# Performance work log

Measured on AMD Instinct MI355X. Metric: run time of the kernel, lower is better.

## Reference

```python
import jax, jax.numpy as jnp
import numpy as np

B, T, L = 64, 512, 48
START, PAD, END = 46, 45, 47


def setup_inputs() -> dict:
    key = jax.random.key(0)
    k1, k2, k3 = jax.random.split(key, 3)
    scores = jax.random.normal(k1, (B, T, L), dtype=jnp.float32)
    gold_target = jax.random.randint(k2, (B, T), 0, L, dtype=jnp.int64)
    trans = jax.random.normal(k3, (L, L), dtype=jnp.float32)
    # replicate the in-place constraint initialization from __init__ (order matters)
    trans = trans.at[:, START].set(-10000.0)
    trans = trans.at[END, :].set(-10000.0)
    trans = trans.at[PAD, :].set(-10000.0)
    trans = trans.at[PAD, END].set(0.0)
    trans = trans.at[PAD, PAD].set(0.0)
    trans = trans.at[START, :].set(0.0)
    mask = jnp.ones((B, T), dtype=jnp.int32)
    return {"scores": scores, "gold_target": gold_target, "mask": mask, "transitions": trans}


def reference(scores, gold_target, mask, transitions):
    Bn, Tn, Ln = scores.shape
    # crf_scores[t, b, from, to] = emission(b, t, from) + transitions[from, to]  (time-major)
    crf = scores.transpose(1, 0, 2)[:, :, :, None] + transitions[None, None]      # (T, B, L, L)
    start = jnp.broadcast_to(transitions[None, None], (1, Bn, Ln, Ln))
    crf = jnp.concatenate([start, crf], axis=0)                                   # (T+1, B, L, L)

    # gold energy: faithful to original torch.gather on flattened (L*L) with raw tag index
    gold = jnp.concatenate(
        [jnp.full((1, Bn), START, dtype=gold_target.dtype), gold_target.T], axis=0)  # (T+1, B)
    flat = crf.reshape(Tn + 1, Bn, Ln * Ln)
    tg = jnp.take_along_axis(flat, gold[:, :, None], axis=2)[:, :, 0]             # (T+1, B)
    maskp = jnp.concatenate([jnp.ones((1, Bn), mask.dtype), mask.T], axis=0)      # (T+1, B)
    tg_energy = jnp.sum(tg * maskp.astype(tg.dtype))

    # forward algorithm (stable log-sum-exp recurrence) via lax.scan
    init = crf[0, :, START, :]                                                    # (B, L)
    def step(fs, xs):
        trans_t, m_t = xs                                                         # (B,L,L), (B,)
        nxt = jax.nn.logsumexp(fs[:, :, None] + trans_t, axis=1)                  # (B, L)
        fs = jnp.where(m_t[:, None].astype(bool), nxt, fs)
        return fs, None
    fs, _ = jax.lax.scan(step, init, (crf[1:], maskp[1:]))
    forscore = fs[:, END].sum()

    return (forscore - tg_energy) / Bn
```

## Files before the change

kernel.cpp:

```cpp
#include <hip/hip_runtime.h>

#define Bn 64
#define Tn 512
#define Ln 48
#define START_L 46
#define PAD_L 45
#define END_L 47
#define QP 72
#define LSEG 16
#define NSEG 8
#define NCHUNK (Tn / (LSEG * NSEG))

typedef __bf16 bf16x8 __attribute__((ext_vector_type(8)));
typedef float f32x4 __attribute__((ext_vector_type(4)));
#define MFMA __builtin_amdgcn_mfma_f32_16x16x32_bf16

__device__ __forceinline__ unsigned short f2bf(float x) {
    unsigned u = __float_as_uint(x);
    u += 0x7fffu + ((u >> 16) & 1u);
    return (unsigned short)(u >> 16);
}
__device__ __forceinline__ unsigned pkT(float a, float b) {
    return __builtin_amdgcn_perm(__float_as_uint(b), __float_as_uint(a), 0x07060302u);
}
__device__ __forceinline__ float bcast0(float x) {
    return __int_as_float(__builtin_amdgcn_readfirstlane(__float_as_int(x)));
}
__device__ __forceinline__ float4 exp4(float4 v) {
    float4 r; r.x = __expf(v.x); r.y = __expf(v.y); r.z = __expf(v.z); r.w = __expf(v.w);
    return r;
}


__device__ __forceinline__ void readTB(const unsigned short* buf, int c, int q, bf16x8 F[3][2]) {
    #pragma unroll
    for (int x = 0; x < 3; ++x) {
        F[x][0] = *(const bf16x8*)&buf[(x * 16 + c) * QP + q * 8];
        F[x][1] = *(const bf16x8*)&buf[(x * 16 + c) * QP + 32 + q * 8];
    }
}

__device__ __forceinline__ void storeTB(unsigned short* buf, int c, int q,
                                        const f32x4 (&acc)[3][3],
                                        float4 w0, float4 w1, float4 w2) {
    #pragma unroll
    for (int nt = 0; nt < 3; ++nt) {
        unsigned u0 = pkT(acc[0][nt][0] * w0.x, acc[0][nt][1] * w0.y);
        unsigned u1 = pkT(acc[0][nt][2] * w0.z, acc[0][nt][3] * w0.w);
        unsigned u2 = pkT(acc[1][nt][0] * w1.x, acc[1][nt][1] * w1.y);
        unsigned u3 = pkT(acc[1][nt][2] * w1.z, acc[1][nt][3] * w1.w);
        unsigned u4 = pkT(acc[2][nt][0] * w2.x, acc[2][nt][1] * w2.y);
        unsigned u5 = pkT(acc[2][nt][2] * w2.z, acc[2][nt][3] * w2.w);
        unsigned short* wp = &buf[(nt * 16 + c) * QP + q * 16];
        uint4 s4; s4.x = u0; s4.y = u1; s4.z = u2; s4.w = u3;
        *(uint4*)wp = s4;
        uint2 s2; s2.x = u4; s2.y = u5;
        *(uint2*)(wp + 8) = s2;
    }
}

__device__ __forceinline__ float treeProd(const unsigned short* bufA, const unsigned short* bufB,
                                          unsigned short* dst, int c, int q) {
    bf16x8 FA[3][2], FB[3][2];
    readTB(bufA, c, q, FA);
    readTB(bufB, c, q, FB);
    f32x4 acc[3][3];
    const f32x4 z = {0.f, 0.f, 0.f, 0.f};
    #pragma unroll
    for (int mt = 0; mt < 3; ++mt)
        #pragma unroll
        for (int nt = 0; nt < 3; ++nt) {
            acc[mt][nt] = MFMA(FA[mt][0], FB[nt][0], z, 0, 0, 0);
            acc[mt][nt] = MFMA(FA[mt][1], FB[nt][1], acc[mt][nt], 0, 0, 0);
        }
    float r = bcast0(acc[0][0][0]);
    float rr = __builtin_amdgcn_rcpf(r);
    float4 w; w.x = rr; w.y = rr; w.z = rr; w.w = rr;
    storeTB(dst, c, q, acc, w, w, w);
    return __logf(r);
}

__global__ __launch_bounds__(512, 2) void scan_k(
        const float* __restrict__ scores,
        const float* __restrict__ trans,
        unsigned short* __restrict__ ws2M,
        float* __restrict__ ws2S,
        float* __restrict__ out) {
    const int b   = blockIdx.x & (Bn - 1);
    const int cid = blockIdx.x >> 6;
    const int tid = threadIdx.x;
    const int w   = tid >> 6;
    const int lane = tid & 63;
    const int c = lane & 15;
    const int q = lane >> 4;

    __shared__ __align__(16) unsigned short TBs[NSEG][48 * QP];
    __shared__ float scl[16];

    for (int i = tid; i < NSEG * 48 * QP / 4; i += 512)
        ((unsigned long long*)TBs)[i] = 0ull;
    __syncthreads();

    const int s    = cid * NSEG + w;
    const int t0   = s * LSEG;
    const int tend = t0 + LSEG - 1;
    const int dirOdd = w & 1;
    const float* sb = scores + (size_t)b * Tn * Ln;

    bf16x8 A[3][2];
    #pragma unroll
    for (int mt = 0; mt < 3; ++mt)
        #pragma unroll
        for (int kt = 0; kt < 2; ++kt) {
            union { unsigned u[4]; bf16x8 v; } fu;
            #pragma unroll
            for (int j2 = 0; j2 < 4; ++j2) {
                int kk0 = kt * 32 + q * 8 + 2 * j2;
                int rem = kk0 & 15;
                if (rem < 12) {
                    int row0 = (rem >> 2) * 16 + (kk0 >> 4) * 4 + (kk0 & 3);
                    float tv0 = dirOdd ? trans[(mt * 16 + c) * Ln + row0]
                                       : trans[row0 * Ln + mt * 16 + c];
                    float tv1 = dirOdd ? trans[(mt * 16 + c) * Ln + row0 + 1]
                                       : trans[(row0 + 1) * Ln + mt * 16 + c];
                    fu.u[j2] = pkT(__expf(tv0), __expf(tv1));
                } else fu.u[j2] = 0u;
            }
            A[mt][kt] = fu.v;
        }

    unsigned short* myTB = TBs[w];

    if (lane < Ln) {
        int m16 = lane >> 4, q4 = (lane >> 2) & 3, r = lane & 3;
        int kk = q4 * 16 + m16 * 4 + r;
        myTB[lane * QP + kk] = dirOdd ? (unsigned short)0x3F80
                                      : f2bf(__expf(sb[(size_t)t0 * Ln + lane]));
    }

    float4 wA, wB, wC, rA, rB, rC;
    {
        int t1 = dirOdd ? tend : (t0 + 1);
        const float* rp = sb + (size_t)t1 * Ln;
        wA = exp4(*(const float4*)(rp + q * 4));
        wB = exp4(*(const float4*)(rp + 16 + q * 4));
        wC = exp4(*(const float4*)(rp + 32 + q * 4));
        int t2 = dirOdd ? (tend - 1) : (t0 + 2);
        const float* rp2 = sb + (size_t)t2 * Ln;
        rA = *(const float4*)(rp2 + q * 4);
        rB = *(const float4*)(rp2 + 16 + q * 4);
        rC = *(const float4*)(rp2 + 32 + q * 4);
    }

    f32x4 acc[3][3];
    float Cs = 0.f;
    for (int tau = 0; tau < LSEG; ++tau) {
        bf16x8 Bf[3][2];
        readTB(myTB, c, q, Bf);

        int tp = dirOdd ? (tend - (tau + 2)) : (t0 + 3 + tau);
        if (tp < t0) tp = t0;
        if (tp > tend) tp = tend;
        const float* rp3 = sb + (size_t)tp * Ln;
        float4 nA = *(const float4*)(rp3 + q * 4);
        float4 nB = *(const float4*)(rp3 + 16 + q * 4);
        float4 nC = *(const float4*)(rp3 + 32 + q * 4);

        const f32x4 z = {0.f, 0.f, 0.f, 0.f};
        #pragma unroll
        for (int mt = 0; mt < 3; ++mt)
            #pragma unroll
            for (int nt = 0; nt < 3; ++nt) {
                acc[mt][nt] = MFMA(A[mt][0], Bf[nt][0], z, 0, 0, 0);
                acc[mt][nt] = MFMA(A[mt][1], Bf[nt][1], acc[mt][nt], 0, 0, 0);
            }

        float4 w0 = wA, w1 = wB, w2 = wC;
        if (!dirOdd && tau == LSEG - 1) {
            w0.x = w0.y = w0.z = w0.w = 1.f; w1 = w0; w2 = w0;
        }
        if ((tau & 3) == 0) {
            float r = bcast0(acc[0][0][0]);
            float rr = __builtin_amdgcn_rcpf(r);
            Cs += __logf(r);
            w0.x *= rr; w0.y *= rr; w0.z *= rr; w0.w *= rr;
            w1.x *= rr; w1.y *= rr; w1.z *= rr; w1.w *= rr;
            w2.x *= rr; w2.y *= rr; w2.z *= rr; w2.w *= rr;
        }
        storeTB(myTB, c, q, acc, w0, w1, w2);

        wA = exp4(rA); wB = exp4(rB); wC = exp4(rC);
        rA = nA; rB = nB; rC = nC;
    }
    if (lane == 0) scl[w] = Cs;
    __syncthreads();

    if (w < 4) {
        const unsigned short* bufA = TBs[(w & 1) ? (2 * w) : (2 * w + 1)];
        const unsigned short* bufB = TBs[(w & 1) ? (2 * w + 1) : (2 * w)];
        float lg = treeProd(bufA, bufB, TBs[2 * w], c, q);
        if (lane == 0) scl[8 + w] = lg;
    }
    __syncthreads();
    if (w < 2) {
        const unsigned short* bufA = TBs[w ? 4 : 2];
        const unsigned short* bufB = TBs[w ? 6 : 0];
        float lg = treeProd(bufA, bufB, TBs[w ? 4 : 0], c, q);
        if (lane == 0) scl[12 + w] = lg;
    }
    __syncthreads();
    if (w == 0) {
        bf16x8 FA[3][2], FB[3][2];
        readTB(TBs[4], c, q, FA);
        readTB(TBs[0], c, q, FB);
        f32x4 pac[3][3];
        const f32x4 z = {0.f, 0.f, 0.f, 0.f};
        #pragma unroll
        for (int mt = 0; mt < 3; ++mt)
            #pragma unroll
            for (int nt = 0; nt < 3; ++nt) {
                pac[mt][nt] = MFMA(FA[mt][0], FB[nt][0], z, 0, 0, 0);
                pac[mt][nt] = MFMA(FA[mt][1], FB[nt][1], pac[mt][nt], 0, 0, 0);
            }
        float r = bcast0(pac[0][0][0]);
        float rr = __builtin_amdgcn_rcpf(r);
        float Ct = __logf(r);
        #pragma unroll
        for (int i2 = 0; i2 < 14; ++i2) Ct += scl[i2];
        unsigned short* mp = ws2M + (size_t)blockIdx.x * (Ln * Ln);
        #pragma unroll
        for (int mt = 0; mt < 3; ++mt)
            #pragma unroll
            for (int nt = 0; nt < 3; ++nt)
                #pragma unroll
                for (int r2 = 0; r2 < 4; ++r2)
                    mp[(mt * 16 + q * 4 + r2) * Ln + nt * 16 + c] = f2bf(pac[mt][nt][r2] * rr);
        if (lane == 0) ws2S[blockIdx.x] = Ct;
    }
    if (blockIdx.x == 0 && tid == 0) out[0] = 0.f;
}

__global__ __launch_bounds__(64) void fin_k(
        const float* __restrict__ scores,
        const int* __restrict__ gold,
        const int* __restrict__ mask,
        const float* __restrict__ trans,
        const unsigned short* __restrict__ ws2M,
        const float* __restrict__ ws2S,
        float* __restrict__ out) {
    const int b = blockIdx.x;
    const int lane = threadIdx.x;
    const int j = (lane < Ln) ? lane : (Ln - 1);

    __shared__ float vB[64];

    float v = (lane < Ln) ? __expf(trans[START_L * Ln + lane]) : 0.0f;
    float Ctot = 0.0f;

    uint4 rows[NCHUNK][6];
    #pragma unroll
    for (int s2 = 0; s2 < NCHUNK; ++s2) {
        const unsigned short* p = ws2M + (size_t)(s2 * Bn + b) * (Ln * Ln) + (size_t)j * Ln;
        #pragma unroll
        for (int k = 0; k < 6; ++k) rows[s2][k] = *(const uint4*)(p + k * 8);
    }

    #pragma unroll
    for (int s2 = 0; s2 < NCHUNK; ++s2) {
        float Cs = ws2S[s2 * Bn + b];
        if (lane < Ln) vB[lane] = v;

        float a0 = 0.f, a1 = 0.f, a2 = 0.f, a3 = 0.f;
        #pragma unroll
        for (int k2 = 0; k2 < 12; ++k2) {
            float4 vb = *(const float4*)&vB[k2 * 4];
            uint4 ch = rows[s2][k2 >> 1];
            unsigned d0 = (k2 & 1) ? ch.z : ch.x;
            unsigned d1 = (k2 & 1) ? ch.w : ch.y;
            float f0 = __uint_as_float(d0 << 16);
            float f1 = __uint_as_float(d0 & 0xffff0000u);
            float f2 = __uint_as_float(d1 << 16);
            float f3 = __uint_as_float(d1 & 0xffff0000u);
            a0 = fmaf(f0, vb.x, a0);
            a1 = fmaf(f1, vb.y, a1);
            a2 = fmaf(f2, vb.z, a2);
            a3 = fmaf(f3, vb.w, a3);
        }
        float accv = (a0 + a1) + (a2 + a3);

        float r = bcast0(accv);
        v = accv * __builtin_amdgcn_rcpf(r);
        Ctot += __logf(r) + Cs;
    }

    if (lane == END_L) {
        atomicAdd(out, (__logf(v) + Ctot) * (1.0f / Bn));
    }

    float tgv = 0.0f;
    #pragma unroll
    for (int k = 0; k < Tn / 64; ++k) {
        int t = lane + k * 64;
        int idx = b * Tn + t;
        if (mask[idx]) tgv += scores[(size_t)idx * Ln] + trans[gold[idx]];
    }
    #pragma unroll
    for (int off = 32; off > 0; off >>= 1) tgv += __shfl_down(tgv, off);
    if (lane == 0) {
        float vv = -tgv * (1.0f / Bn);
        if (b == 0) vv -= trans[START_L];
        atomicAdd(out, vv);
    }
}

extern "C" void kernel_launch(void* const* d_in, const int* in_sizes, int n_in,
                              void* d_out, int out_size, void* d_ws, size_t ws_size,
                              hipStream_t stream) {
    const float* scores = (const float*)d_in[0];
    const int*   gold   = (const int*)d_in[1];
    const int*   mask   = (const int*)d_in[2];
    const float* trans  = (const float*)d_in[3];
    float* out = (float*)d_out;

    unsigned short* ws2M = (unsigned short*)d_ws;
    float* ws2S = (float*)((char*)d_ws + (size_t)Bn * NCHUNK * Ln * Ln * 2);

    scan_k<<<Bn * NCHUNK, 512, 0, stream>>>(scores, trans, ws2M, ws2S, out);
    fin_k<<<Bn, 64, 0, stream>>>(scores, gold, mask, trans, ws2M, ws2S, out);
}
```

Measured before the change: 85.43 us.

## Add prep kernel to precompute exponentiated emissions, transition fragments and gold terms

```diff
diff --git a/kernel.cpp b/kernel.cpp
--- a/kernel.cpp
+++ b/kernel.cpp
@@ -15,6 +15,11 @@
 typedef float f32x4 __attribute__((ext_vector_type(4)));
 #define MFMA __builtin_amdgcn_mfma_f32_16x16x32_bf16
 
+#define OFF_2M (6291456)
+#define OFF_A  (OFF_2M + 1179648)
+#define OFF_G  (OFF_A + 12288)
+#define OFF_2S (OFF_G + 131072)
+
 __device__ __forceinline__ unsigned short f2bf(float x) {
     unsigned u = __float_as_uint(x);
     u += 0x7fffu + ((u >> 16) & 1u);
@@ -29,6 +34,56 @@
 __device__ __forceinline__ float4 exp4(float4 v) {
     float4 r; r.x = __expf(v.x); r.y = __expf(v.y); r.z = __expf(v.z); r.w = __expf(v.w);
     return r;
+}
+
+__global__ __launch_bounds__(256) void prep_k(
+        const float* __restrict__ scores,
+        const int* __restrict__ gold,
+        const float* __restrict__ trans,
+        float* __restrict__ wsE,
+        float* __restrict__ wsG,
+        uint4* __restrict__ wsA,
+        float* __restrict__ out) {
+    const int gid = blockIdx.x * 256 + threadIdx.x;
+    const int gsz = gridDim.x * 256;
+
+    const int N4 = Bn * Tn * Ln / 4;
+    for (int i = gid; i < N4; i += gsz) {
+        float4 v = ((const float4*)scores)[i];
+        ((float4*)wsE)[i] = exp4(v);
+    }
+
+    for (int i = gid; i < Bn * Tn; i += gsz) {
+        wsG[i] = scores[(size_t)i * Ln] + trans[gold[i]];
+    }
+
+    if (blockIdx.x == 0) {
+        for (int e = threadIdx.x; e < 768; e += 256) {
+            int lane = e & 63;
+            int kt   = (e >> 6) & 1;
+            int mt   = (e >> 7) % 3;
+            int dir  = e >= 384;
+            int c = lane & 15, q = lane >> 4;
+            uint4 val;
+            unsigned uu[4];
+            #pragma unroll
+            for (int j2 = 0; j2 < 4; ++j2) {
+                int kk0 = kt * 32 + q * 8 + 2 * j2;
+                int rem = kk0 & 15;
+                if (rem < 12) {
+                    int row0 = (rem >> 2) * 16 + (kk0 >> 4) * 4 + (kk0 & 3);
+                    float tv0 = dir ? trans[(mt * 16 + c) * Ln + row0]
+                                    : trans[row0 * Ln + mt * 16 + c];
+                    float tv1 = dir ? trans[(mt * 16 + c) * Ln + row0 + 1]
+                                    : trans[(row0 + 1) * Ln + mt * 16 + c];
+                    uu[j2] = pkT(__expf(tv0), __expf(tv1));
+                } else uu[j2] = 0u;
+            }
+            val.x = uu[0]; val.y = uu[1]; val.z = uu[2]; val.w = uu[3];
+            wsA[e] = val;
+        }
+        if (threadIdx.x == 255) out[0] = 0.0f;
+    }
 }
 
 
@@ -81,11 +136,10 @@
 }
 
 __global__ __launch_bounds__(512, 2) void scan_k(
-        const float* __restrict__ scores,
-        const float* __restrict__ trans,
+        const float* __restrict__ wsE,
+        const uint4* __restrict__ wsA,
         unsigned short* __restrict__ ws2M,
-        float* __restrict__ ws2S,
-        float* __restrict__ out) {
+        float* __restrict__ ws2S) {
     const int b   = blockIdx.x & (Bn - 1);
     const int cid = blockIdx.x >> 6;
     const int tid = threadIdx.x;
@@ -105,29 +159,20 @@
     const int t0   = s * LSEG;
     const int tend = t0 + LSEG - 1;
     const int dirOdd = w & 1;
-    const float* sb = scores + (size_t)b * Tn * Ln;
+    const float* eb = wsE + (size_t)b * Tn * Ln;
 
     bf16x8 A[3][2];
-    #pragma unroll
-    for (int mt = 0; mt < 3; ++mt)
-        #pragma unroll
-        for (int kt = 0; kt < 2; ++kt) {
-            union { unsigned u[4]; bf16x8 v; } fu;
-            #pragma unroll
-            for (int j2 = 0; j2 < 4; ++j2) {
-                int kk0 = kt * 32 + q * 8 + 2 * j2;
-                int rem = kk0 & 15;
-                if (rem < 12) {
-                    int row0 = (rem >> 2) * 16 + (kk0 >> 4) * 4 + (kk0 & 3);
-                    float tv0 = dirOdd ? trans[(mt * 16 + c) * Ln + row0]
-                                       : trans[row0 * Ln + mt * 16 + c];
-                    float tv1 = dirOdd ? trans[(mt * 16 + c) * Ln + row0 + 1]
-                                       : trans[(row0 + 1) * Ln + mt * 16 + c];
-                    fu.u[j2] = pkT(__expf(tv0), __expf(tv1));
-                } else fu.u[j2] = 0u;
+    {
+        const uint4* ap = wsA + (dirOdd ? 384 : 0) + lane;
+        #pragma unroll
+        for (int mt = 0; mt < 3; ++mt)
+            #pragma unroll
+            for (int kt = 0; kt < 2; ++kt) {
+                union { uint4 u; bf16x8 v; } fu;
+                fu.u = ap[(mt * 2 + kt) * 64];
+                A[mt][kt] = fu.v;
             }
-            A[mt][kt] = fu.v;
-        }
+    }
 
     unsigned short* myTB = TBs[w];
 
@@ -135,18 +180,18 @@
         int m16 = lane >> 4, q4 = (lane >> 2) & 3, r = lane & 3;
         int kk = q4 * 16 + m16 * 4 + r;
         myTB[lane * QP + kk] = dirOdd ? (unsigned short)0x3F80
-                                      : f2bf(__expf(sb[(size_t)t0 * Ln + lane]));
+                                      : f2bf(eb[(size_t)t0 * Ln + lane]);
     }
 
     float4 wA, wB, wC, rA, rB, rC;
     {
         int t1 = dirOdd ? tend : (t0 + 1);
-        const float* rp = sb + (size_t)t1 * Ln;
-        wA = exp4(*(const float4*)(rp + q * 4));
-        wB = exp4(*(const float4*)(rp + 16 + q * 4));
-        wC = exp4(*(const float4*)(rp + 32 + q * 4));
+        const float* rp = eb + (size_t)t1 * Ln;
+        wA = *(const float4*)(rp + q * 4);
+        wB = *(const float4*)(rp + 16 + q * 4);
+        wC = *(const float4*)(rp + 32 + q * 4);
         int t2 = dirOdd ? (tend - 1) : (t0 + 2);
-        const float* rp2 = sb + (size_t)t2 * Ln;
+        const float* rp2 = eb + (size_t)t2 * Ln;
         rA = *(const float4*)(rp2 + q * 4);
         rB = *(const float4*)(rp2 + 16 + q * 4);
         rC = *(const float4*)(rp2 + 32 + q * 4);
@@ -161,7 +206,7 @@
         int tp = dirOdd ? (tend - (tau + 2)) : (t0 + 3 + tau);
         if (tp < t0) tp = t0;
         if (tp > tend) tp = tend;
-        const float* rp3 = sb + (size_t)tp * Ln;
+        const float* rp3 = eb + (size_t)tp * Ln;
         float4 nA = *(const float4*)(rp3 + q * 4);
         float4 nB = *(const float4*)(rp3 + 16 + q * 4);
         float4 nC = *(const float4*)(rp3 + 32 + q * 4);
@@ -189,7 +234,7 @@
         }
         storeTB(myTB, c, q, acc, w0, w1, w2);
 
-        wA = exp4(rA); wB = exp4(rB); wC = exp4(rC);
+        wA = rA; wB = rB; wC = rC;
         rA = nA; rB = nB; rC = nC;
     }
     if (lane == 0) scl[w] = Cs;
@@ -237,16 +282,14 @@
                     mp[(mt * 16 + q * 4 + r2) * Ln + nt * 16 + c] = f2bf(pac[mt][nt][r2] * rr);
         if (lane == 0) ws2S[blockIdx.x] = Ct;
     }
-    if (blockIdx.x == 0 && tid == 0) out[0] = 0.f;
 }
 
 __global__ __launch_bounds__(64) void fin_k(
-        const float* __restrict__ scores,
-        const int* __restrict__ gold,
         const int* __restrict__ mask,
         const float* __restrict__ trans,
         const unsigned short* __restrict__ ws2M,
         const float* __restrict__ ws2S,
+        const float* __restrict__ wsG,
         float* __restrict__ out) {
     const int b = blockIdx.x;
     const int lane = threadIdx.x;
@@ -300,9 +343,8 @@
     float tgv = 0.0f;
     #pragma unroll
     for (int k = 0; k < Tn / 64; ++k) {
-        int t = lane + k * 64;
-        int idx = b * Tn + t;
-        if (mask[idx]) tgv += scores[(size_t)idx * Ln] + trans[gold[idx]];
+        int idx = b * Tn + lane + k * 64;
+        if (mask[idx]) tgv += wsG[idx];
     }
     #pragma unroll
     for (int off = 32; off > 0; off >>= 1) tgv += __shfl_down(tgv, off);
@@ -322,9 +364,14 @@
     const float* trans  = (const float*)d_in[3];
     float* out = (float*)d_out;
 
-    unsigned short* ws2M = (unsigned short*)d_ws;
-    float* ws2S = (float*)((char*)d_ws + (size_t)Bn * NCHUNK * Ln * Ln * 2);
-
-    scan_k<<<Bn * NCHUNK, 512, 0, stream>>>(scores, trans, ws2M, ws2S, out);
-    fin_k<<<Bn, 64, 0, stream>>>(scores, gold, mask, trans, ws2M, ws2S, out);
-}
+    char* base = (char*)d_ws;
+    float*          wsE  = (float*)base;
+    unsigned short* ws2M = (unsigned short*)(base + OFF_2M);
+    uint4*          wsA  = (uint4*)(base + OFF_A);
+    float*          wsG  = (float*)(base + OFF_G);
+    float*          ws2S = (float*)(base + OFF_2S);
+
+    prep_k<<<512, 256, 0, stream>>>(scores, gold, trans, wsE, wsG, wsA, out);
+    scan_k<<<Bn * NCHUNK, 512, 0, stream>>>(wsE, wsA, ws2M, ws2S);
+    fin_k<<<Bn, 64, 0, stream>>>(mask, trans, ws2M, ws2S, wsG, out);
+}
```

Measured after the change: 88.97 us. 4.1% more time.

## Interleave two independent segment chains per wave with shorter segments

Applied to the files above, without the earlier changes.

```diff
diff --git a/kernel.cpp b/kernel.cpp
--- a/kernel.cpp
+++ b/kernel.cpp
@@ -7,9 +7,9 @@
 #define PAD_L 45
 #define END_L 47
 #define QP 72
-#define LSEG 16
-#define NSEG 8
-#define NCHUNK (Tn / (LSEG * NSEG))
+#define LSEG 8
+#define NBUF 16
+#define NCHUNK (Tn / (LSEG * NBUF))
 
 typedef __bf16 bf16x8 __attribute__((ext_vector_type(8)));
 typedef float f32x4 __attribute__((ext_vector_type(4)));
@@ -94,17 +94,18 @@
     const int c = lane & 15;
     const int q = lane >> 4;
 
-    __shared__ __align__(16) unsigned short TBs[NSEG][48 * QP];
-    __shared__ float scl[16];
-
-    for (int i = tid; i < NSEG * 48 * QP / 4; i += 512)
+    __shared__ __align__(16) unsigned short TBs[NBUF][48 * QP];
+    __shared__ float scl[32];
+
+    for (int i = tid; i < NBUF * 48 * QP / 4; i += 512)
         ((unsigned long long*)TBs)[i] = 0ull;
     __syncthreads();
 
-    const int s    = cid * NSEG + w;
-    const int t0   = s * LSEG;
-    const int tend = t0 + LSEG - 1;
     const int dirOdd = w & 1;
+    const int s1 = cid * NBUF + w;
+    const int s2 = s1 + 8;
+    const int t0a = s1 * LSEG, tea = t0a + LSEG - 1;
+    const int t0b = s2 * LSEG, teb = t0b + LSEG - 1;
     const float* sb = scores + (size_t)b * Tn * Ln;
 
     bf16x8 A[3][2];
@@ -129,89 +130,130 @@
             A[mt][kt] = fu.v;
         }
 
-    unsigned short* myTB = TBs[w];
+    unsigned short* TB0 = TBs[w];
+    unsigned short* TB1 = TBs[w + 8];
 
     if (lane < Ln) {
         int m16 = lane >> 4, q4 = (lane >> 2) & 3, r = lane & 3;
         int kk = q4 * 16 + m16 * 4 + r;
-        myTB[lane * QP + kk] = dirOdd ? (unsigned short)0x3F80
-                                      : f2bf(__expf(sb[(size_t)t0 * Ln + lane]));
-    }
-
-    float4 wA, wB, wC, rA, rB, rC;
+        TB0[lane * QP + kk] = dirOdd ? (unsigned short)0x3F80
+                                     : f2bf(__expf(sb[(size_t)t0a * Ln + lane]));
+        TB1[lane * QP + kk] = dirOdd ? (unsigned short)0x3F80
+                                     : f2bf(__expf(sb[(size_t)t0b * Ln + lane]));
+    }
+
+    auto clampA = [&](int t) { return t < t0a ? t0a : (t > tea ? tea : t); };
+    auto clampB = [&](int t) { return t < t0b ? t0b : (t > teb ? teb : t); };
+
+    float4 wA0, wA1, wA2, wB0, wB1, wB2;
     {
-        int t1 = dirOdd ? tend : (t0 + 1);
-        const float* rp = sb + (size_t)t1 * Ln;
-        wA = exp4(*(const float4*)(rp + q * 4));
-        wB = exp4(*(const float4*)(rp + 16 + q * 4));
-        wC = exp4(*(const float4*)(rp + 32 + q * 4));
-        int t2 = dirOdd ? (tend - 1) : (t0 + 2);
-        const float* rp2 = sb + (size_t)t2 * Ln;
-        rA = *(const float4*)(rp2 + q * 4);
-        rB = *(const float4*)(rp2 + 16 + q * 4);
-        rC = *(const float4*)(rp2 + 32 + q * 4);
-    }
-
-    f32x4 acc[3][3];
-    float Cs = 0.f;
+        const float* rp = sb + (size_t)(dirOdd ? tea : (t0a + 1)) * Ln;
+        wA0 = exp4(*(const float4*)(rp + q * 4));
+        wA1 = exp4(*(const float4*)(rp + 16 + q * 4));
+        wA2 = exp4(*(const float4*)(rp + 32 + q * 4));
+        const float* rp2 = sb + (size_t)(dirOdd ? teb : (t0b + 1)) * Ln;
+        wB0 = exp4(*(const float4*)(rp2 + q * 4));
+        wB1 = exp4(*(const float4*)(rp2 + 16 + q * 4));
+        wB2 = exp4(*(const float4*)(rp2 + 32 + q * 4));
+    }
+
+    f32x4 acc0[3][3], acc1[3][3];
+    float Cs0 = 0.f, Cs1 = 0.f;
     for (int tau = 0; tau < LSEG; ++tau) {
-        bf16x8 Bf[3][2];
-        readTB(myTB, c, q, Bf);
-
-        int tp = dirOdd ? (tend - (tau + 2)) : (t0 + 3 + tau);
-        if (tp < t0) tp = t0;
-        if (tp > tend) tp = tend;
-        const float* rp3 = sb + (size_t)tp * Ln;
-        float4 nA = *(const float4*)(rp3 + q * 4);
-        float4 nB = *(const float4*)(rp3 + 16 + q * 4);
-        float4 nC = *(const float4*)(rp3 + 32 + q * 4);
+        bf16x8 Bf0[3][2], Bf1[3][2];
+        readTB(TB0, c, q, Bf0);
+        readTB(TB1, c, q, Bf1);
+
+        int tnA = clampA(dirOdd ? (tea - (tau + 1)) : (t0a + 2 + tau));
+        int tnB = clampB(dirOdd ? (teb - (tau + 1)) : (t0b + 2 + tau));
+        const float* rpA = sb + (size_t)tnA * Ln;
+        const float* rpB = sb + (size_t)tnB * Ln;
+        float4 nA0 = *(const float4*)(rpA + q * 4);
+        float4 nA1 = *(const float4*)(rpA + 16 + q * 4);
+        float4 nA2 = *(const float4*)(rpA + 32 + q * 4);
+        float4 nB0 = *(const float4*)(rpB + q * 4);
+        float4 nB1 = *(const float4*)(rpB + 16 + q * 4);
+        float4 nB2 = *(const float4*)(rpB + 32 + q * 4);
 
         const f32x4 z = {0.f, 0.f, 0.f, 0.f};
         #pragma unroll
         for (int mt = 0; mt < 3; ++mt)
             #pragma unroll
             for (int nt = 0; nt < 3; ++nt) {
-                acc[mt][nt] = MFMA(A[mt][0], Bf[nt][0], z, 0, 0, 0);
-                acc[mt][nt] = MFMA(A[mt][1], Bf[nt][1], acc[mt][nt], 0, 0, 0);
-            }
-
-        float4 w0 = wA, w1 = wB, w2 = wC;
-        if (!dirOdd && tau == LSEG - 1) {
-            w0.x = w0.y = w0.z = w0.w = 1.f; w1 = w0; w2 = w0;
-        }
-        if ((tau & 3) == 0) {
-            float r = bcast0(acc[0][0][0]);
-            float rr = __builtin_amdgcn_rcpf(r);
-            Cs += __logf(r);
-            w0.x *= rr; w0.y *= rr; w0.z *= rr; w0.w *= rr;
-            w1.x *= rr; w1.y *= rr; w1.z *= rr; w1.w *= rr;
-            w2.x *= rr; w2.y *= rr; w2.z *= rr; w2.w *= rr;
-        }
-        storeTB(myTB, c, q, acc, w0, w1, w2);
-
-        wA = exp4(rA); wB = exp4(rB); wC = exp4(rC);
-        rA = nA; rB = nB; rC = nC;
-    }
-    if (lane == 0) scl[w] = Cs;
-    __syncthreads();
-
+                acc0[mt][nt] = MFMA(A[mt][0], Bf0[nt][0], z, 0, 0, 0);
+                acc0[mt][nt] = MFMA(A[mt][1], Bf0[nt][1], acc0[mt][nt], 0, 0, 0);
+            }
+        #pragma unroll
+        for (int mt = 0; mt < 3; ++mt)
+            #pragma unroll
+            for (int nt = 0; nt < 3; ++nt) {
+                acc1[mt][nt] = MFMA(A[mt][0], Bf1[nt][0], z, 0, 0, 0);
+                acc1[mt][nt] = MFMA(A[mt][1], Bf1[nt][1], acc1[mt][nt], 0, 0, 0);
+            }
+
+        const bool lastEven = (!dirOdd && tau == LSEG - 1);
+        const bool doRenorm = (tau & 3) == 0;
+
+        {
+            float4 w0 = wA0, w1 = wA1, w2 = wA2;
+            if (lastEven) { w0.x = w0.y = w0.z = w0.w = 1.f; w1 = w0; w2 = w0; }
+            if (doRenorm) {
+                float r = bcast0(acc0[0][0][0]);
+                float rr = __builtin_amdgcn_rcpf(r);
+                Cs0 += __logf(r);
+                w0.x *= rr; w0.y *= rr; w0.z *= rr; w0.w *= rr;
+                w1.x *= rr; w1.y *= rr; w1.z *= rr; w1.w *= rr;
+                w2.x *= rr; w2.y *= rr; w2.z *= rr; w2.w *= rr;
+            }
+            storeTB(TB0, c, q, acc0, w0, w1, w2);
+        }
+        {
+            float4 w0 = wB0, w1 = wB1, w2 = wB2;
+            if (lastEven) { w0.x = w0.y = w0.z = w0.w = 1.f; w1 = w0; w2 = w0; }
+            if (doRenorm) {
+                float r = bcast0(acc1[0][0][0]);
+                float rr = __builtin_amdgcn_rcpf(r);
+                Cs1 += __logf(r);
+                w0.x *= rr; w0.y *= rr; w0.z *= rr; w0.w *= rr;
+                w1.x *= rr; w1.y *= rr; w1.z *= rr; w1.w *= rr;
+                w2.x *= rr; w2.y *= rr; w2.z *= rr; w2.w *= rr;
+            }
+            storeTB(TB1, c, q, acc1, w0, w1, w2);
+        }
+
+        wA0 = exp4(nA0); wA1 = exp4(nA1); wA2 = exp4(nA2);
+        wB0 = exp4(nB0); wB1 = exp4(nB1); wB2 = exp4(nB2);
+    }
+    if (lane == 0) { scl[w] = Cs0; scl[w + 8] = Cs1; }
+    __syncthreads();
+
+    {
+        int i = w;
+        const unsigned short* bufA = TBs[2 * i + ((i & 1) ? 0 : 1)];
+        const unsigned short* bufB = TBs[2 * i + ((i & 1) ? 1 : 0)];
+        float lg = treeProd(bufA, bufB, TBs[2 * i], c, q);
+        if (lane == 0) scl[16 + i] = lg;
+    }
+    __syncthreads();
     if (w < 4) {
-        const unsigned short* bufA = TBs[(w & 1) ? (2 * w) : (2 * w + 1)];
-        const unsigned short* bufB = TBs[(w & 1) ? (2 * w + 1) : (2 * w)];
-        float lg = treeProd(bufA, bufB, TBs[2 * w], c, q);
-        if (lane == 0) scl[8 + w] = lg;
+        int j = w;
+        const unsigned short* bufA = TBs[4 * j + ((j & 1) ? 0 : 2)];
+        const unsigned short* bufB = TBs[4 * j + ((j & 1) ? 2 : 0)];
+        float lg = treeProd(bufA, bufB, TBs[4 * j], c, q);
+        if (lane == 0) scl[24 + j] = lg;
     }
     __syncthreads();
     if (w < 2) {
-        const unsigned short* bufA = TBs[w ? 4 : 2];
-        const unsigned short* bufB = TBs[w ? 6 : 0];
-        float lg = treeProd(bufA, bufB, TBs[w ? 4 : 0], c, q);
-        if (lane == 0) scl[12 + w] = lg;
+        int p = w;
+        const unsigned short* bufA = TBs[8 * p + ((p & 1) ? 0 : 4)];
+        const unsigned short* bufB = TBs[8 * p + ((p & 1) ? 4 : 0)];
+        float lg = treeProd(bufA, bufB, TBs[8 * p], c, q);
+        if (lane == 0) scl[28 + p] = lg;
     }
     __syncthreads();
     if (w == 0) {
         bf16x8 FA[3][2], FB[3][2];
-        readTB(TBs[4], c, q, FA);
+        readTB(TBs[8], c, q, FA);
         readTB(TBs[0], c, q, FB);
         f32x4 pac[3][3];
         const f32x4 z = {0.f, 0.f, 0.f, 0.f};
@@ -226,7 +268,7 @@
         float rr = __builtin_amdgcn_rcpf(r);
         float Ct = __logf(r);
         #pragma unroll
-        for (int i2 = 0; i2 < 14; ++i2) Ct += scl[i2];
+        for (int i2 = 0; i2 < 30; ++i2) Ct += scl[i2];
         unsigned short* mp = ws2M + (size_t)blockIdx.x * (Ln * Ln);
         #pragma unroll
         for (int mt = 0; mt < 3; ++mt)
```

Result: slower. 90.09 us (+5.4%).
